# Optimization experiments

Measured on AMD Instinct MI355X. Metric: run time of the kernel, lower is better.

Reference implementation:

```python
import jax, jax.numpy as jnp
import numpy as np
from jax import lax

B, T, IN, H, OUT = 256, 1024, 128, 10, 128


def setup_inputs() -> dict:
    key = jax.random.key(0)
    ks = jax.random.split(key, 12)
    s_in = 1.0 / np.sqrt(H)  # PyTorch RNN init scale U(-1/sqrt(H), 1/sqrt(H))
    u = lambda k, shp: jax.random.uniform(k, shp, jnp.float32, -s_in, s_in)
    return {
        "x": jax.random.normal(ks[0], (B, T, IN), jnp.float32),
        "W_ih0": u(ks[1], (H, IN)),
        "W_hh0": u(ks[2], (H, H)),
        "b_ih0": u(ks[3], (H,)),
        "b_hh0": u(ks[4], (H,)),
        "W_ih1": u(ks[5], (H, H)),
        "W_hh1": u(ks[6], (H, H)),
        "b_ih1": u(ks[7], (H,)),
        "b_hh1": u(ks[8], (H,)),
        "W_lin": u(ks[9], (OUT, H)),
        "b_lin": u(ks[10], (OUT,)),
    }


def _rnn_layer(x_seq, W_ih, W_hh, b_ih, b_hh):
    # x_seq: [B, T, F]. Precompute input projection once (big GEMM),
    # then scan the tiny recurrent update over time.
    xp = jnp.einsum('btf,hf->bth', x_seq, W_ih) + b_ih + b_hh  # [B, T, H]
    h0 = jnp.zeros((x_seq.shape[0], W_hh.shape[0]), x_seq.dtype)

    def step(h, xt):  # xt: [B, H]
        h_new = jax.nn.relu(xt + h @ W_hh.T)
        return h_new, h_new

    hT, ys = lax.scan(step, h0, xp.transpose(1, 0, 2))  # ys: [T, B, H]
    return ys.transpose(1, 0, 2), hT


def reference(x, W_ih0, W_hh0, b_ih0, b_hh0, W_ih1, W_hh1, b_ih1, b_hh1, W_lin, b_lin):
    out1, h1 = _rnn_layer(x, W_ih0, W_hh0, b_ih0, b_hh0)
    out2, h2 = _rnn_layer(out1, W_ih1, W_hh1, b_ih1, b_hh1)
    logits = jnp.einsum('bth,oh->bto', out2, W_lin) + b_lin  # [B, T, OUT]
    out = jax.nn.softmax(logits, axis=-1)
    hidden = jnp.stack([h1, h2], axis=0)  # [num_layers, B, H]
    return out, hidden
```

## Files before the change

kernel.cpp:

```cpp
#include <hip/hip_runtime.h>

#define Bn   256
#define Tn   1024
#define INn  128
#define Hn   10
#define OUTn 128
#define BTn  (Bn * Tn)

__global__ __launch_bounds__(256) void k1_inproj(
    const float* __restrict__ x,
    const float* __restrict__ Wih0,
    const float* __restrict__ bih0,
    const float* __restrict__ bhh0,
    float* __restrict__ xp0)
{
    __shared__ float Ws[Hn][INn];
    __shared__ float bs[16];
    const int tid = threadIdx.x;
    for (int idx = tid; idx < Hn * INn / 4; idx += 256)
        reinterpret_cast<float4*>(&Ws[0][0])[idx] =
            reinterpret_cast<const float4*>(Wih0)[idx];
    if (tid < 16) bs[tid] = (tid < Hn) ? (bih0[tid] + bhh0[tid]) : 0.f;
    __syncthreads();

    const int row = blockIdx.x * 256 + tid;
    const float4* xr = reinterpret_cast<const float4*>(x + (size_t)row * INn);

    float acc[Hn];
    #pragma unroll
    for (int j = 0; j < Hn; ++j) acc[j] = bs[j];

    #pragma unroll
    for (int c = 0; c < INn / 4; ++c) {
        float4 v = xr[c];
        #pragma unroll
        for (int j = 0; j < Hn; ++j) {
            const float4 w = *reinterpret_cast<const float4*>(&Ws[j][c * 4]);
            acc[j] = fmaf(v.x, w.x, acc[j]);
            acc[j] = fmaf(v.y, w.y, acc[j]);
            acc[j] = fmaf(v.z, w.z, acc[j]);
            acc[j] = fmaf(v.w, w.w, acc[j]);
        }
    }
    float4* op = reinterpret_cast<float4*>(xp0 + (size_t)row * 16);
    op[0] = make_float4(acc[0], acc[1], acc[2], acc[3]);
    op[1] = make_float4(acc[4], acc[5], acc[6], acc[7]);
    op[2] = make_float4(acc[8], acc[9], 0.f, 0.f);
    op[3] = make_float4(0.f, 0.f, 0.f, 0.f);
}

static __device__ __forceinline__ void pinv(float& v) {
    asm volatile("" : "+v"(v));
}
#define SWZB(v, k) __int_as_float(__builtin_amdgcn_ds_swizzle(__float_as_int(v), ((k) << 5)))

#define RSTEP(XV, YV) do {                                                                  \
    const float sa0=SWZB(vh,0),  sa1=SWZB(vh,1),  sa2=SWZB(vh,2),  sa3=SWZB(vh,3);          \
    const float sa4=SWZB(vh,4),  sa5=SWZB(vh,5),  sa6=SWZB(vh,6),  sa7=SWZB(vh,7);          \
    const float sa8=SWZB(vh,8),  sa9=SWZB(vh,9);                                            \
    const float sb0=SWZB(vh,16), sb1=SWZB(vh,17), sb2=SWZB(vh,18), sb3=SWZB(vh,19);         \
    const float sb4=SWZB(vh,20), sb5=SWZB(vh,21), sb6=SWZB(vh,22), sb7=SWZB(vh,23);         \
    const float sb8=SWZB(vh,24), sb9=SWZB(vh,25);                                           \
    float c0 = half ? biasv : (XV);                                                         \
    float c1 = 0.f, c2 = 0.f, c3 = 0.f;                                                     \
    c0 = fmaf(A0, sa0, c0); c1 = fmaf(A1, sa1, c1); c2 = fmaf(A2, sa2, c2); c3 = fmaf(A3, sa3, c3); \
    c0 = fmaf(A4, sa4, c0); c1 = fmaf(A5, sa5, c1); c2 = fmaf(A6, sa6, c2); c3 = fmaf(A7, sa7, c3); \
    c0 = fmaf(A8, sa8, c0); c1 = fmaf(A9, sa9, c1); c2 = fmaf(B0, sb0, c2); c3 = fmaf(B1, sb1, c3); \
    c0 = fmaf(B2, sb2, c0); c1 = fmaf(B3, sb3, c1); c2 = fmaf(B4, sb4, c2); c3 = fmaf(B5, sb5, c3); \
    c0 = fmaf(B6, sb6, c0); c1 = fmaf(B7, sb7, c1); c2 = fmaf(B8, sb8, c2); c3 = fmaf(B9, sb9, c3); \
    const float hn_ = fmaxf((c0 + c1) + (c2 + c3), 0.f);                                    \
    vh = hn_; (YV) = hn_;                                                                   \
} while (0)

__global__ __launch_bounds__(64, 1) void k2_recur(
    const float* __restrict__ xp0,
    const float* __restrict__ Whh0,
    const float* __restrict__ Wih1,
    const float* __restrict__ Whh1,
    const float* __restrict__ bih1,
    const float* __restrict__ bhh1,
    float* __restrict__ h2seq,
    float* __restrict__ hidden)
{
    const int lane = threadIdx.x;
    if (lane >= 32) return;
    const int half = lane >> 4;
    const int j    = lane & 15;
    const int jc   = (j < Hn) ? j : (Hn - 1);
    const int b    = blockIdx.x;

    const float* Arow = half ? (Wih1 + jc * Hn) : (Whh0 + jc * Hn);
    const float* Brow = half ? (Whh1 + jc * Hn) : (Whh0 + jc * Hn);
    float A0 = Arow[0], A1 = Arow[1], A2 = Arow[2], A3 = Arow[3], A4 = Arow[4];
    float A5 = Arow[5], A6 = Arow[6], A7 = Arow[7], A8 = Arow[8], A9 = Arow[9];
    float B0 = Brow[0], B1 = Brow[1], B2 = Brow[2], B3 = Brow[3], B4 = Brow[4];
    float B5 = Brow[5], B6 = Brow[6], B7 = Brow[7], B8 = Brow[8], B9 = Brow[9];
    if (!half) { B0=B1=B2=B3=B4=B5=B6=B7=B8=B9=0.f; }
    float biasv = bih1[jc] + bhh1[jc];

    pinv(A0); pinv(A1); pinv(A2); pinv(A3); pinv(A4);
    pinv(A5); pinv(A6); pinv(A7); pinv(A8); pinv(A9);
    pinv(B0); pinv(B1); pinv(B2); pinv(B3); pinv(B4);
    pinv(B5); pinv(B6); pinv(B7); pinv(B8); pinv(B9);
    pinv(biasv);

    const bool st = half && (j < Hn);
    const bool s1 = !half && (j < Hn);

    const float* xp = xp0 + (size_t)b * Tn * 16 + j;
    float*       h2w = h2seq + (size_t)b * Tn * Hn + j;

    float x0 = xp[0*16],  x1 = xp[1*16],  x2 = xp[2*16],  x3 = xp[3*16];
    float x4 = xp[4*16],  x5 = xp[5*16],  x6 = xp[6*16],  x7 = xp[7*16];
    float x8 = xp[8*16],  x9 = xp[9*16],  x10 = xp[10*16], x11 = xp[11*16];
    float x12 = xp[12*16], x13 = xp[13*16], x14 = xp[14*16], x15 = xp[15*16];

    float vh = half ? 0.f : fmaxf(x0, 0.f);
    x0 = xp[16*16];

    float y0, y1, y2, y3, y4, y5, y6, y7;

    RSTEP(x1, y1); x1 = xp[17*16];
    RSTEP(x2, y2); x2 = xp[18*16];
    RSTEP(x3, y3); x3 = xp[19*16];
    RSTEP(x4, y4); x4 = xp[20*16];
    RSTEP(x5, y5); x5 = xp[21*16];
    RSTEP(x6, y6); x6 = xp[22*16];
    RSTEP(x7, y7); x7 = xp[23*16];
    if (st) {
        h2w[0]  = y1; h2w[10] = y2; h2w[20] = y3; h2w[30] = y4;
        h2w[40] = y5; h2w[50] = y6; h2w[60] = y7;
    }
    xp += 128; h2w += 70;

    #define BLK_LO() do {                                   \
        RSTEP(x0, y0); x0 = xp[16*16];                      \
        RSTEP(x1, y1); x1 = xp[17*16];                      \
        RSTEP(x2, y2); x2 = xp[18*16];                      \
        RSTEP(x3, y3); x3 = xp[19*16];                      \
        RSTEP(x4, y4); x4 = xp[20*16];                      \
        RSTEP(x5, y5); x5 = xp[21*16];                      \
        RSTEP(x6, y6); x6 = xp[22*16];                      \
        RSTEP(x7, y7); x7 = xp[23*16];                      \
        if (st) {                                           \
            h2w[0]  = y0; h2w[10] = y1; h2w[20] = y2; h2w[30] = y3; \
            h2w[40] = y4; h2w[50] = y5; h2w[60] = y6; h2w[70] = y7; \
        }                                                   \
        xp += 128; h2w += 80;                               \
    } while (0)
    #define BLK_HI() do {                                   \
        RSTEP(x8,  y0); x8  = xp[16*16];                    \
        RSTEP(x9,  y1); x9  = xp[17*16];                    \
        RSTEP(x10, y2); x10 = xp[18*16];                    \
        RSTEP(x11, y3); x11 = xp[19*16];                    \
        RSTEP(x12, y4); x12 = xp[20*16];                    \
        RSTEP(x13, y5); x13 = xp[21*16];                    \
        RSTEP(x14, y6); x14 = xp[22*16];                    \
        RSTEP(x15, y7); x15 = xp[23*16];                    \
        if (st) {                                           \
            h2w[0]  = y0; h2w[10] = y1; h2w[20] = y2; h2w[30] = y3; \
            h2w[40] = y4; h2w[50] = y5; h2w[60] = y6; h2w[70] = y7; \
        }                                                   \
        xp += 128; h2w += 80;                               \
    } while (0)

    for (int p = 0; p < 63; ++p) {
        BLK_HI();
        BLK_LO();
    }
    BLK_HI();

    const float h1fin = vh;
    float yfin;
    RSTEP(0.f, yfin);
    if (st) {
        h2w[0] = yfin;
        hidden[Bn * Hn + b * Hn + (lane - 16)] = yfin;
    }
    if (s1) {
        hidden[b * Hn + lane] = h1fin;
    }
    #undef BLK_LO
    #undef BLK_HI
}

__global__ __launch_bounds__(256) void k3_outproj(
    const float* __restrict__ h2seq,
    const float* __restrict__ Wlin,
    const float* __restrict__ blin,
    float* __restrict__ out)
{
    const int lane = threadIdx.x & 63;
    const int wid  = blockIdx.x * 4 + (threadIdx.x >> 6);
    const int g    = lane >> 4;
    const int i    = lane & 15;

    float wl[8][Hn], bl[8];
    #pragma unroll
    for (int s = 0; s < 8; ++s) {
        const int o = i * 8 + s;
        bl[s] = blin[o];
        #pragma unroll
        for (int k = 0; k < Hn; ++k) wl[s][k] = Wlin[o * Hn + k];
    }

    for (int r = wid * 4 + g; r < BTn; r += 4096 * 4) {
        const float hv = (i < Hn) ? h2seq[(size_t)r * Hn + i] : 0.f;
        float acc[8];
        #pragma unroll
        for (int s = 0; s < 8; ++s) acc[s] = bl[s];
        #pragma unroll
        for (int k = 0; k < Hn; ++k) {
            const float hk = __shfl(hv, k, 16);
            #pragma unroll
            for (int s = 0; s < 8; ++s) acc[s] = fmaf(wl[s][k], hk, acc[s]);
        }
        float m = acc[0];
        #pragma unroll
        for (int s = 1; s < 8; ++s) m = fmaxf(m, acc[s]);
        #pragma unroll
        for (int off = 1; off < 16; off <<= 1) m = fmaxf(m, __shfl_xor(m, off, 16));
        float e[8], ssum = 0.f;
        #pragma unroll
        for (int s = 0; s < 8; ++s) { e[s] = __expf(acc[s] - m); ssum += e[s]; }
        #pragma unroll
        for (int off = 1; off < 16; off <<= 1) ssum += __shfl_xor(ssum, off, 16);
        const float inv = 1.0f / ssum;
        float4* op = reinterpret_cast<float4*>(out + (size_t)r * OUTn + i * 8);
        op[0] = make_float4(e[0] * inv, e[1] * inv, e[2] * inv, e[3] * inv);
        op[1] = make_float4(e[4] * inv, e[5] * inv, e[6] * inv, e[7] * inv);
    }
}

extern "C" void kernel_launch(void* const* d_in, const int* in_sizes, int n_in,
                              void* d_out, int out_size, void* d_ws, size_t ws_size,
                              hipStream_t stream)
{
    const float* x    = (const float*)d_in[0];
    const float* Wih0 = (const float*)d_in[1];
    const float* Whh0 = (const float*)d_in[2];
    const float* bih0 = (const float*)d_in[3];
    const float* bhh0 = (const float*)d_in[4];
    const float* Wih1 = (const float*)d_in[5];
    const float* Whh1 = (const float*)d_in[6];
    const float* bih1 = (const float*)d_in[7];
    const float* bhh1 = (const float*)d_in[8];
    const float* Wlin = (const float*)d_in[9];
    const float* blin = (const float*)d_in[10];

    float* out    = (float*)d_out;
    float* hidden = out + (size_t)BTn * OUTn;

    float* xp0   = (float*)d_ws;
    float* h2seq = xp0 + (size_t)BTn * 16;

    k1_inproj<<<BTn / 256, 256, 0, stream>>>(x, Wih0, bih0, bhh0, xp0);
    k2_recur<<<Bn, 64, 0, stream>>>(xp0, Whh0, Wih1, Whh1, bih1, bhh1, h2seq, hidden);
    k3_outproj<<<1024, 256, 0, stream>>>(h2seq, Wlin, blin, out);
}
```

Measured before the change: 431.4 us.

## Pack four batches per wave in recurrence using DPP row rotations

```diff
diff --git a/kernel.cpp b/kernel.cpp
--- a/kernel.cpp
+++ b/kernel.cpp
@@ -52,24 +52,62 @@
 static __device__ __forceinline__ void pinv(float& v) {
     asm volatile("" : "+v"(v));
 }
-#define SWZB(v, k) __int_as_float(__builtin_amdgcn_ds_swizzle(__float_as_int(v), ((k) << 5)))
-
-#define RSTEP(XV, YV) do {                                                                  \
-    const float sa0=SWZB(vh,0),  sa1=SWZB(vh,1),  sa2=SWZB(vh,2),  sa3=SWZB(vh,3);          \
-    const float sa4=SWZB(vh,4),  sa5=SWZB(vh,5),  sa6=SWZB(vh,6),  sa7=SWZB(vh,7);          \
-    const float sa8=SWZB(vh,8),  sa9=SWZB(vh,9);                                            \
-    const float sb0=SWZB(vh,16), sb1=SWZB(vh,17), sb2=SWZB(vh,18), sb3=SWZB(vh,19);         \
-    const float sb4=SWZB(vh,20), sb5=SWZB(vh,21), sb6=SWZB(vh,22), sb7=SWZB(vh,23);         \
-    const float sb8=SWZB(vh,24), sb9=SWZB(vh,25);                                           \
-    float c0 = half ? biasv : (XV);                                                         \
-    float c1 = 0.f, c2 = 0.f, c3 = 0.f;                                                     \
-    c0 = fmaf(A0, sa0, c0); c1 = fmaf(A1, sa1, c1); c2 = fmaf(A2, sa2, c2); c3 = fmaf(A3, sa3, c3); \
-    c0 = fmaf(A4, sa4, c0); c1 = fmaf(A5, sa5, c1); c2 = fmaf(A6, sa6, c2); c3 = fmaf(A7, sa7, c3); \
-    c0 = fmaf(A8, sa8, c0); c1 = fmaf(A9, sa9, c1); c2 = fmaf(B0, sb0, c2); c3 = fmaf(B1, sb1, c3); \
-    c0 = fmaf(B2, sb2, c0); c1 = fmaf(B3, sb3, c1); c2 = fmaf(B4, sb4, c2); c3 = fmaf(B5, sb5, c3); \
-    c0 = fmaf(B6, sb6, c0); c1 = fmaf(B7, sb7, c1); c2 = fmaf(B8, sb8, c2); c3 = fmaf(B9, sb9, c3); \
-    const float hn_ = fmaxf((c0 + c1) + (c2 + c3), 0.f);                                    \
-    vh = hn_; (YV) = hn_;                                                                   \
+#define ROTR(v, R) __int_as_float(__builtin_amdgcn_mov_dpp(__float_as_int(v), 0x120 + (R), 0xf, 0xf, false))
+
+#define STEP(XV, YV) do {                                               \
+    float d0 = biasv, d1 = 0.f, d2 = 0.f, d3 = 0.f;                     \
+    d0 = fmaf(vh2,          Wb0,  d0);                                  \
+    d1 = fmaf(ROTR(vh2, 1), Wb1,  d1);                                  \
+    d2 = fmaf(ROTR(vh2, 2), Wb2,  d2);                                  \
+    d3 = fmaf(ROTR(vh2, 3), Wb3,  d3);                                  \
+    d0 = fmaf(ROTR(vh2, 4), Wb4,  d0);                                  \
+    d1 = fmaf(ROTR(vh2, 5), Wb5,  d1);                                  \
+    d2 = fmaf(ROTR(vh2, 6), Wb6,  d2);                                  \
+    d3 = fmaf(ROTR(vh2, 7), Wb7,  d3);                                  \
+    d0 = fmaf(ROTR(vh2, 8), Wb8,  d0);                                  \
+    d1 = fmaf(ROTR(vh2, 9), Wb9,  d1);                                  \
+    d2 = fmaf(ROTR(vh2,10), Wb10, d2);                                  \
+    d3 = fmaf(ROTR(vh2,11), Wb11, d3);                                  \
+    d0 = fmaf(ROTR(vh2,12), Wb12, d0);                                  \
+    d1 = fmaf(ROTR(vh2,13), Wb13, d1);                                  \
+    d2 = fmaf(ROTR(vh2,14), Wb14, d2);                                  \
+    d3 = fmaf(ROTR(vh2,15), Wb15, d3);                                  \
+    float c0 = (XV), c1 = 0.f, c2 = 0.f, c3 = 0.f;                      \
+    c0 = fmaf(vh1,          Wa0,  c0);                                  \
+    c1 = fmaf(ROTR(vh1, 1), Wa1,  c1);                                  \
+    c2 = fmaf(ROTR(vh1, 2), Wa2,  c2);                                  \
+    c3 = fmaf(ROTR(vh1, 3), Wa3,  c3);                                  \
+    c0 = fmaf(ROTR(vh1, 4), Wa4,  c0);                                  \
+    c1 = fmaf(ROTR(vh1, 5), Wa5,  c1);                                  \
+    c2 = fmaf(ROTR(vh1, 6), Wa6,  c2);                                  \
+    c3 = fmaf(ROTR(vh1, 7), Wa7,  c3);                                  \
+    c0 = fmaf(ROTR(vh1, 8), Wa8,  c0);                                  \
+    c1 = fmaf(ROTR(vh1, 9), Wa9,  c1);                                  \
+    c2 = fmaf(ROTR(vh1,10), Wa10, c2);                                  \
+    c3 = fmaf(ROTR(vh1,11), Wa11, c3);                                  \
+    c0 = fmaf(ROTR(vh1,12), Wa12, c0);                                  \
+    c1 = fmaf(ROTR(vh1,13), Wa13, c1);                                  \
+    c2 = fmaf(ROTR(vh1,14), Wa14, c2);                                  \
+    c3 = fmaf(ROTR(vh1,15), Wa15, c3);                                  \
+    const float h1n = fmaxf((c0 + c1) + (c2 + c3), 0.f);                \
+    d0 = fmaf(h1n,          Wc0,  d0);                                  \
+    d1 = fmaf(ROTR(h1n, 1), Wc1,  d1);                                  \
+    d2 = fmaf(ROTR(h1n, 2), Wc2,  d2);                                  \
+    d3 = fmaf(ROTR(h1n, 3), Wc3,  d3);                                  \
+    d0 = fmaf(ROTR(h1n, 4), Wc4,  d0);                                  \
+    d1 = fmaf(ROTR(h1n, 5), Wc5,  d1);                                  \
+    d2 = fmaf(ROTR(h1n, 6), Wc6,  d2);                                  \
+    d3 = fmaf(ROTR(h1n, 7), Wc7,  d3);                                  \
+    d0 = fmaf(ROTR(h1n, 8), Wc8,  d0);                                  \
+    d1 = fmaf(ROTR(h1n, 9), Wc9,  d1);                                  \
+    d2 = fmaf(ROTR(h1n,10), Wc10, d2);                                  \
+    d3 = fmaf(ROTR(h1n,11), Wc11, d3);                                  \
+    d0 = fmaf(ROTR(h1n,12), Wc12, d0);                                  \
+    d1 = fmaf(ROTR(h1n,13), Wc13, d1);                                  \
+    d2 = fmaf(ROTR(h1n,14), Wc14, d2);                                  \
+    d3 = fmaf(ROTR(h1n,15), Wc15, d3);                                  \
+    const float h2n = fmaxf((d0 + d1) + (d2 + d3), 0.f);                \
+    vh1 = h1n; vh2 = h2n; (YV) = h2n;                                   \
 } while (0)
 
 __global__ __launch_bounds__(64, 1) void k2_recur(
@@ -83,105 +121,94 @@
     float* __restrict__ hidden)
 {
     const int lane = threadIdx.x;
-    if (lane >= 32) return;
-    const int half = lane >> 4;
-    const int j    = lane & 15;
-    const int jc   = (j < Hn) ? j : (Hn - 1);
-    const int b    = blockIdx.x;
-
-    const float* Arow = half ? (Wih1 + jc * Hn) : (Whh0 + jc * Hn);
-    const float* Brow = half ? (Whh1 + jc * Hn) : (Whh0 + jc * Hn);
-    float A0 = Arow[0], A1 = Arow[1], A2 = Arow[2], A3 = Arow[3], A4 = Arow[4];
-    float A5 = Arow[5], A6 = Arow[6], A7 = Arow[7], A8 = Arow[8], A9 = Arow[9];
-    float B0 = Brow[0], B1 = Brow[1], B2 = Brow[2], B3 = Brow[3], B4 = Brow[4];
-    float B5 = Brow[5], B6 = Brow[6], B7 = Brow[7], B8 = Brow[8], B9 = Brow[9];
-    if (!half) { B0=B1=B2=B3=B4=B5=B6=B7=B8=B9=0.f; }
-    float biasv = bih1[jc] + bhh1[jc];
-
-    pinv(A0); pinv(A1); pinv(A2); pinv(A3); pinv(A4);
-    pinv(A5); pinv(A6); pinv(A7); pinv(A8); pinv(A9);
-    pinv(B0); pinv(B1); pinv(B2); pinv(B3); pinv(B4);
-    pinv(B5); pinv(B6); pinv(B7); pinv(B8); pinv(B9);
+    const int jl   = lane & 15;
+    const int row  = lane >> 4;
+    const int b    = blockIdx.x * 4 + row;
+
+    const int delta = (__builtin_amdgcn_mov_dpp(jl, 0x121, 0xf, 0xf, false) - jl) & 15;
+
+    const bool okj  = (jl < Hn);
+    const int  jrow = (okj ? jl : 0) * Hn;
+
+    float Wa0,Wa1,Wa2,Wa3,Wa4,Wa5,Wa6,Wa7,Wa8,Wa9,Wa10,Wa11,Wa12,Wa13,Wa14,Wa15;
+    float Wb0,Wb1,Wb2,Wb3,Wb4,Wb5,Wb6,Wb7,Wb8,Wb9,Wb10,Wb11,Wb12,Wb13,Wb14,Wb15;
+    float Wc0,Wc1,Wc2,Wc3,Wc4,Wc5,Wc6,Wc7,Wc8,Wc9,Wc10,Wc11,Wc12,Wc13,Wc14,Wc15;
+
+    #define LDW(R) do {                                                 \
+        const int  kk = (jl + (R) * delta) & 15;                        \
+        const bool v  = okj && (kk < Hn);                               \
+        const int  ii = jrow + (v ? kk : 0);                            \
+        Wa##R = v ? Whh0[ii] : 0.f;                                     \
+        Wb##R = v ? Whh1[ii] : 0.f;                                     \
+        Wc##R = v ? Wih1[ii] : 0.f;                                     \
+    } while (0)
+    LDW(0);  LDW(1);  LDW(2);  LDW(3);  LDW(4);  LDW(5);  LDW(6);  LDW(7);
+    LDW(8);  LDW(9);  LDW(10); LDW(11); LDW(12); LDW(13); LDW(14); LDW(15);
+    #undef LDW
+
+    float biasv = okj ? (bih1[jl] + bhh1[jl]) : 0.f;
+
+    pinv(Wa0); pinv(Wa1); pinv(Wa2); pinv(Wa3); pinv(Wa4); pinv(Wa5); pinv(Wa6); pinv(Wa7);
+    pinv(Wa8); pinv(Wa9); pinv(Wa10); pinv(Wa11); pinv(Wa12); pinv(Wa13); pinv(Wa14); pinv(Wa15);
+    pinv(Wb0); pinv(Wb1); pinv(Wb2); pinv(Wb3); pinv(Wb4); pinv(Wb5); pinv(Wb6); pinv(Wb7);
+    pinv(Wb8); pinv(Wb9); pinv(Wb10); pinv(Wb11); pinv(Wb12); pinv(Wb13); pinv(Wb14); pinv(Wb15);
+    pinv(Wc0); pinv(Wc1); pinv(Wc2); pinv(Wc3); pinv(Wc4); pinv(Wc5); pinv(Wc6); pinv(Wc7);
+    pinv(Wc8); pinv(Wc9); pinv(Wc10); pinv(Wc11); pinv(Wc12); pinv(Wc13); pinv(Wc14); pinv(Wc15);
     pinv(biasv);
 
-    const bool st = half && (j < Hn);
-    const bool s1 = !half && (j < Hn);
-
-    const float* xp = xp0 + (size_t)b * Tn * 16 + j;
-    float*       h2w = h2seq + (size_t)b * Tn * Hn + j;
+    const float* xp  = xp0 + (size_t)b * Tn * 16 + jl;
+    float*       h2w = h2seq + (size_t)b * Tn * Hn + jl;
 
     float x0 = xp[0*16],  x1 = xp[1*16],  x2 = xp[2*16],  x3 = xp[3*16];
     float x4 = xp[4*16],  x5 = xp[5*16],  x6 = xp[6*16],  x7 = xp[7*16];
     float x8 = xp[8*16],  x9 = xp[9*16],  x10 = xp[10*16], x11 = xp[11*16];
     float x12 = xp[12*16], x13 = xp[13*16], x14 = xp[14*16], x15 = xp[15*16];
 
-    float vh = half ? 0.f : fmaxf(x0, 0.f);
-    x0 = xp[16*16];
-
+    float vh1 = 0.f, vh2 = 0.f;
     float y0, y1, y2, y3, y4, y5, y6, y7;
 
-    RSTEP(x1, y1); x1 = xp[17*16];
-    RSTEP(x2, y2); x2 = xp[18*16];
-    RSTEP(x3, y3); x3 = xp[19*16];
-    RSTEP(x4, y4); x4 = xp[20*16];
-    RSTEP(x5, y5); x5 = xp[21*16];
-    RSTEP(x6, y6); x6 = xp[22*16];
-    RSTEP(x7, y7); x7 = xp[23*16];
-    if (st) {
-        h2w[0]  = y1; h2w[10] = y2; h2w[20] = y3; h2w[30] = y4;
-        h2w[40] = y5; h2w[50] = y6; h2w[60] = y7;
-    }
-    xp += 128; h2w += 70;
-
     #define BLK_LO() do {                                   \
-        RSTEP(x0, y0); x0 = xp[16*16];                      \
-        RSTEP(x1, y1); x1 = xp[17*16];                      \
-        RSTEP(x2, y2); x2 = xp[18*16];                      \
-        RSTEP(x3, y3); x3 = xp[19*16];                      \
-        RSTEP(x4, y4); x4 = xp[20*16];                      \
-        RSTEP(x5, y5); x5 = xp[21*16];                      \
-        RSTEP(x6, y6); x6 = xp[22*16];                      \
-        RSTEP(x7, y7); x7 = xp[23*16];                      \
-        if (st) {                                           \
+        STEP(x0, y0); x0 = xp[16*16];                       \
+        STEP(x1, y1); x1 = xp[17*16];                       \
+        STEP(x2, y2); x2 = xp[18*16];                       \
+        STEP(x3, y3); x3 = xp[19*16];                       \
+        STEP(x4, y4); x4 = xp[20*16];                       \
+        STEP(x5, y5); x5 = xp[21*16];                       \
+        STEP(x6, y6); x6 = xp[22*16];                       \
+        STEP(x7, y7); x7 = xp[23*16];                       \
+        if (okj) {                                          \
             h2w[0]  = y0; h2w[10] = y1; h2w[20] = y2; h2w[30] = y3; \
             h2w[40] = y4; h2w[50] = y5; h2w[60] = y6; h2w[70] = y7; \
         }                                                   \
         xp += 128; h2w += 80;                               \
     } while (0)
     #define BLK_HI() do {                                   \
-        RSTEP(x8,  y0); x8  = xp[16*16];                    \
-        RSTEP(x9,  y1); x9  = xp[17*16];                    \
-        RSTEP(x10, y2); x10 = xp[18*16];                    \
-        RSTEP(x11, y3); x11 = xp[19*16];                    \
-        RSTEP(x12, y4); x12 = xp[20*16];                    \
-        RSTEP(x13, y5); x13 = xp[21*16];                    \
-        RSTEP(x14, y6); x14 = xp[22*16];                    \
-        RSTEP(x15, y7); x15 = xp[23*16];                    \
-        if (st) {                                           \
+        STEP(x8,  y0); x8  = xp[16*16];                     \
+        STEP(x9,  y1); x9  = xp[17*16];                     \
+        STEP(x10, y2); x10 = xp[18*16];                     \
+        STEP(x11, y3); x11 = xp[19*16];                     \
+        STEP(x12, y4); x12 = xp[20*16];                     \
+        STEP(x13, y5); x13 = xp[21*16];                     \
+        STEP(x14, y6); x14 = xp[22*16];                     \
+        STEP(x15, y7); x15 = xp[23*16];                     \
+        if (okj) {                                          \
             h2w[0]  = y0; h2w[10] = y1; h2w[20] = y2; h2w[30] = y3; \
             h2w[40] = y4; h2w[50] = y5; h2w[60] = y6; h2w[70] = y7; \
         }                                                   \
         xp += 128; h2w += 80;                               \
     } while (0)
 
-    for (int p = 0; p < 63; ++p) {
+    for (int p = 0; p < 64; ++p) {
+        BLK_LO();
         BLK_HI();
-        BLK_LO();
-    }
-    BLK_HI();
-
-    const float h1fin = vh;
-    float yfin;
-    RSTEP(0.f, yfin);
-    if (st) {
-        h2w[0] = yfin;
-        hidden[Bn * Hn + b * Hn + (lane - 16)] = yfin;
-    }
-    if (s1) {
-        hidden[b * Hn + lane] = h1fin;
     }
     #undef BLK_LO
     #undef BLK_HI
+
+    if (okj) {
+        hidden[b * Hn + jl]           = vh1;
+        hidden[Bn * Hn + b * Hn + jl] = vh2;
+    }
 }
 
 __global__ __launch_bounds__(256) void k3_outproj(
@@ -255,6 +282,6 @@
     float* h2seq = xp0 + (size_t)BTn * 16;
 
     k1_inproj<<<BTn / 256, 256, 0, stream>>>(x, Wih0, bih0, bhh0, xp0);
-    k2_recur<<<Bn, 64, 0, stream>>>(xp0, Whh0, Wih1, Whh1, bih1, bhh1, h2seq, hidden);
+    k2_recur<<<Bn / 4, 64, 0, stream>>>(xp0, Whh0, Wih1, Whh1, bih1, bhh1, h2seq, hidden);
     k3_outproj<<<1024, 256, 0, stream>>>(h2seq, Wlin, blin, out);
 }
```

Measured after the change: 455.1 us. 1.06x slower.
